# Performance work log

Hardware: AMD Instinct MI355X
Metric: run time of the kernel (lower is better)

## Reference

```python
import jax, jax.numpy as jnp
import numpy as np

H = 4        # nhead
TEMP = 0.1   # temperature
TOP_K = 5
SHAPE_EPS = 1e-5


def _ln(x, g, b):
    m = x.mean(-1, keepdims=True)
    v = ((x - m) ** 2).mean(-1, keepdims=True)
    return (x - m) / jnp.sqrt(v + SHAPE_EPS) * g + b


def _mha(x, Wqkv, bqkv, Wo, bo):
    B, L, D = x.shape
    Dh = D // H
    qkv = x @ Wqkv.T + bqkv                     # [B,L,3D]
    q, k, v = jnp.split(qkv, 3, axis=-1)
    q = q.reshape(B, L, H, Dh)
    k = k.reshape(B, L, H, Dh)
    v = v.reshape(B, L, H, Dh)
    att = jnp.einsum('bqhd,bkhd->bhqk', q, k) * (1.0 / np.sqrt(Dh))
    att = jax.nn.softmax(att, axis=-1)
    o = jnp.einsum('bhqk,bkhd->bqhd', att, v).reshape(B, L, D)
    return o @ Wo.T + bo


def _pattern_encoder(x, cls_token, Wqkv, bqkv, Wo, bo, ln1_g, ln1_b,
                     W1, b1, W2, b2, ln2_g, ln2_b, proj_W, proj_b, proj_g, proj_bb):
    B, L, D = x.shape
    h = jnp.concatenate([jnp.broadcast_to(cls_token, (B, 1, D)), x], axis=1)  # [B,L+1,D]
    for i in range(Wqkv.shape[0]):  # num_layers=2, post-norm (PyTorch default)
        a = _mha(h, Wqkv[i], bqkv[i], Wo[i], bo[i])
        h = _ln(h + a, ln1_g[i], ln1_b[i])
        f = jax.nn.gelu(h @ W1[i].T + b1[i], approximate=False) @ W2[i].T + b2[i]
        h = _ln(h + f, ln2_g[i], ln2_b[i])
    cls_out = h[:, 0, :]
    return _ln(cls_out @ proj_W.T + proj_b, proj_g, proj_bb)  # [B,d_repr]


def _value_encoder(xm, vW1, vb1, v_g, v_b, vW2, vb2):
    hh = _ln(xm @ vW1.T + vb1, v_g, v_b)
    return jax.nn.gelu(hh, approximate=False) @ vW2.T + vb2


def setup_inputs() -> dict:
    B, L, D, DR, N, P, NL = 64, 512, 512, 128, 10000, 96, 2
    key = jax.random.key(0)
    ks = jax.random.split(key, 16)
    sc = 0.02
    inp = {
        'query': jax.random.normal(ks[0], (B, L, D), jnp.float32),
        'memory_keys': jax.random.normal(ks[1], (N, DR), jnp.float32),
        'memory_values': jax.random.normal(ks[2], (N, P, D), jnp.float32),
        'cls_token': jax.random.normal(ks[3], (1, 1, D), jnp.float32) * sc,
        'Wqkv': jax.random.normal(ks[4], (NL, 3 * D, D), jnp.float32) * sc,
        'bqkv': jnp.zeros((NL, 3 * D), jnp.float32),
        'Wo': jax.random.normal(ks[5], (NL, D, D), jnp.float32) * sc,
        'bo': jnp.zeros((NL, D), jnp.float32),
        'ln1_g': jnp.ones((NL, D), jnp.float32),
        'ln1_b': jnp.zeros((NL, D), jnp.float32),
        'W1': jax.random.normal(ks[6], (NL, 2 * D, D), jnp.float32) * sc,
        'b1': jnp.zeros((NL, 2 * D), jnp.float32),
        'W2': jax.random.normal(ks[7], (NL, D, 2 * D), jnp.float32) * sc,
        'b2': jnp.zeros((NL, D), jnp.float32),
        'ln2_g': jnp.ones((NL, D), jnp.float32),
        'ln2_b': jnp.zeros((NL, D), jnp.float32),
        'proj_W': jax.random.normal(ks[8], (DR, D), jnp.float32) * sc,
        'proj_b': jnp.zeros((DR,), jnp.float32),
        'proj_g': jnp.ones((DR,), jnp.float32),
        'proj_bb': jnp.zeros((DR,), jnp.float32),
        'vW1': jax.random.normal(ks[9], (DR, D), jnp.float32) * sc,
        'vb1': jnp.zeros((DR,), jnp.float32),
        'v_g': jnp.ones((DR,), jnp.float32),
        'v_b': jnp.zeros((DR,), jnp.float32),
        'vW2': jax.random.normal(ks[10], (DR, DR), jnp.float32) * sc,
        'vb2': jnp.zeros((DR,), jnp.float32),
        'shape_w': jnp.float32(0.5),
    }
    return inp


def reference(query, memory_keys, memory_values, cls_token, Wqkv, bqkv, Wo, bo,
              ln1_g, ln1_b, W1, b1, W2, b2, ln2_g, ln2_b,
              proj_W, proj_b, proj_g, proj_bb, vW1, vb1, v_g, v_b, vW2, vb2, shape_w):
    q_repr = _pattern_encoder(query, cls_token, Wqkv, bqkv, Wo, bo, ln1_g, ln1_b,
                              W1, b1, W2, b2, ln2_g, ln2_b, proj_W, proj_b, proj_g, proj_bb)
    q_val = _value_encoder(query.mean(axis=1), vW1, vb1, v_g, v_b, vW2, vb2)
    qk = shape_w * q_repr + (1.0 - shape_w) * q_val              # [B,DR]
    # squared euclidean distance, expanded form (same math as sum((a-b)^2))
    d = ((qk ** 2).sum(-1)[:, None]
         - 2.0 * qk @ memory_keys.T
         + (memory_keys ** 2).sum(-1)[None, :])                  # [B,N]
    sim = -d / TEMP
    top_scores, top_idx = jax.lax.top_k(sim, TOP_K)              # [B,K]
    weights = jax.nn.softmax(top_scores, axis=-1)
    retrieved = memory_values[top_idx]                           # [B,K,P,D]
    return retrieved, weights
```

## Files before the change

### kernel.cpp

```cpp
#include <hip/hip_runtime.h>
#include <math.h>

#define B_    64
#define LQ    512
#define LC    513
#define DD    512
#define HH    4
#define DH    128
#define DRr   128
#define NKEYS 10000
#define PP    96
#define TOPK  5
#define MROWS (B_*LC)
#define VTSTRIDE 544

typedef __attribute__((ext_vector_type(8))) short short8v;
typedef __attribute__((ext_vector_type(4))) float f32x4;
typedef __attribute__((ext_vector_type(16))) float f32x16;

static __device__ __forceinline__ float gelu_exact(float x) {
    return 0.5f * x * (1.0f + erff(x * 0.70710678118654752440f));
}

static __device__ __forceinline__ unsigned short f2bf(float x) {
    union { float f; unsigned u; } v; v.f = x;
    unsigned r = v.u + 0x7fff + ((v.u >> 16) & 1);
    return (unsigned short)(r >> 16);
}
static __device__ __forceinline__ float bf2f(unsigned short h) {
    union { float f; unsigned u; } v; v.u = ((unsigned)h) << 16;
    return v.f;
}
static __device__ __forceinline__ void split_bf(float x, unsigned short& hi, unsigned short& lo) {
    hi = f2bf(x);
    lo = f2bf(x - bf2f(hi));
}

static __device__ __forceinline__ int xcd_swz(int orig, int nwg) {
    int xcd = orig & 7;
    int lid = orig >> 3;
    int q = nwg >> 3, r = nwg & 7;
    int base = (xcd < r) ? xcd * (q + 1) : r * (q + 1) + (xcd - r) * q;
    return base + lid;
}

static __device__ __forceinline__ void gload16(const unsigned short* g, unsigned short* l) {
    __builtin_amdgcn_global_load_lds(
        (const __attribute__((address_space(1))) unsigned*)g,
        (__attribute__((address_space(3))) unsigned*)l, 16, 0, 0);
}

__global__ __launch_bounds__(256)
void split_kernel(const float* __restrict__ x, unsigned short* __restrict__ hi,
                  unsigned short* __restrict__ lo, int n4)
{
    int i = blockIdx.x * blockDim.x + threadIdx.x;
    if (i >= n4) return;
    float4 v = ((const float4*)x)[i];
    unsigned short h0,h1,h2,h3,l0,l1,l2,l3;
    split_bf(v.x,h0,l0); split_bf(v.y,h1,l1); split_bf(v.z,h2,l2); split_bf(v.w,h3,l3);
    ((uint2*)hi)[i] = make_uint2((unsigned)h0 | ((unsigned)h1 << 16), (unsigned)h2 | ((unsigned)h3 << 16));
    ((uint2*)lo)[i] = make_uint2((unsigned)l0 | ((unsigned)l1 << 16), (unsigned)l2 | ((unsigned)l3 << 16));
}

__global__ __launch_bounds__(256)
void concat_cls(const float* __restrict__ query, const float* __restrict__ cls,
                float* __restrict__ h, unsigned short* __restrict__ h_hi,
                unsigned short* __restrict__ h_lo)
{
    int row = blockIdx.x * 4 + (threadIdx.x >> 6);
    int lane = threadIdx.x & 63;
    int b = row / LC, r = row - b * LC;
    const float* src = (r == 0) ? (cls + lane * 8)
                                : (query + ((size_t)b * LQ + (r - 1)) * DD + lane * 8);
    float4 v0 = *(const float4*)src;
    float4 v1 = *(const float4*)(src + 4);
    size_t o = (size_t)row * DD + lane * 8;
    *(float4*)(h + o) = v0;
    *(float4*)(h + o + 4) = v1;
    float vv[8] = {v0.x,v0.y,v0.z,v0.w,v1.x,v1.y,v1.z,v1.w};
    unsigned short hs[8], ls[8];
    #pragma unroll
    for (int i = 0; i < 8; i++) split_bf(vv[i], hs[i], ls[i]);
    uint4 hv, lv;
    hv.x = (unsigned)hs[0] | ((unsigned)hs[1] << 16);
    hv.y = (unsigned)hs[2] | ((unsigned)hs[3] << 16);
    hv.z = (unsigned)hs[4] | ((unsigned)hs[5] << 16);
    hv.w = (unsigned)hs[6] | ((unsigned)hs[7] << 16);
    lv.x = (unsigned)ls[0] | ((unsigned)ls[1] << 16);
    lv.y = (unsigned)ls[2] | ((unsigned)ls[3] << 16);
    lv.z = (unsigned)ls[4] | ((unsigned)ls[5] << 16);
    lv.w = (unsigned)ls[6] | ((unsigned)ls[7] << 16);
    *(uint4*)(h_hi + o) = hv;
    *(uint4*)(h_lo + o) = lv;
}

#define BM 128
#define BN 128
#define BK 32

#define MFMA32(a, b, c) __builtin_amdgcn_mfma_f32_32x32x16_bf16(a, b, c, 0, 0, 0)

template<int MODE>
__global__ __launch_bounds__(256)
void gemm3(const unsigned short* __restrict__ Ahi, const unsigned short* __restrict__ Alo,
           const unsigned short* __restrict__ Whi, const unsigned short* __restrict__ Wlo,
           const float* __restrict__ bias, const float* __restrict__ res,
           float* __restrict__ Cf, unsigned short* __restrict__ Chi,
           unsigned short* __restrict__ Clo, unsigned* __restrict__ Vix,
           int M, int N, int K, int NBN)
{
    __shared__ __align__(16) unsigned short POOL[16384];

    const int t = threadIdx.x;
    const int lane = t & 63, w = t >> 6;
    const int wr = w >> 1, wc = w & 1;
    const int wg = xcd_swz(blockIdx.x, gridDim.x);
    const int bm = wg / NBN, bn = wg - bm * NBN;
    const int row0 = bm * BM, col0 = bn * BN;

    const int srow = t >> 2;
    const int sg   = t & 3;
    const int glog = sg ^ (srow & 3);
    int ar0 = row0 + srow;      if (ar0 >= M) ar0 = M - 1;
    int ar1 = row0 + srow + 64; if (ar1 >= M) ar1 = M - 1;
    const size_t aoff0 = (size_t)ar0 * K + glog * 8;
    const size_t aoff1 = (size_t)ar1 * K + glog * 8;
    const size_t boff0 = (size_t)(col0 + srow) * K + glog * 8;
    const size_t boff1 = (size_t)(col0 + srow + 64) * K + glog * 8;
    const int ldso0 = t * 8;
    const int ldso1 = t * 8 + 2048;

    f32x16 acc[2][2];
    #pragma unroll
    for (int m = 0; m < 2; m++)
        #pragma unroll
        for (int n = 0; n < 2; n++)
            #pragma unroll
            for (int i = 0; i < 16; i++) acc[m][n][i] = 0.f;

    const int cl = lane & 31;
    const int kg = lane >> 5;
    const int cl3 = cl & 3;

    unsigned short* LAh = POOL;
    unsigned short* LAl = POOL + 4096;
    unsigned short* LBh = POOL + 8192;
    unsigned short* LBl = POOL + 12288;

    const int KT = K / BK;
    for (int kt = 0; kt < KT; kt++) {
        const int k0 = kt * BK;
        __syncthreads();
        gload16(Ahi + aoff0 + k0, &LAh[ldso0]);
        gload16(Ahi + aoff1 + k0, &LAh[ldso1]);
        gload16(Alo + aoff0 + k0, &LAl[ldso0]);
        gload16(Alo + aoff1 + k0, &LAl[ldso1]);
        gload16(Whi + boff0 + k0, &LBh[ldso0]);
        gload16(Whi + boff1 + k0, &LBh[ldso1]);
        gload16(Wlo + boff0 + k0, &LBl[ldso0]);
        gload16(Wlo + boff1 + k0, &LBl[ldso1]);
        __syncthreads();

        #pragma unroll
        for (int ks = 0; ks < 2; ks++) {
            const int blkswz = ((ks * 2 + kg) ^ cl3) * 8;
            short8v ah[2], al[2], bh[2], bl[2];
            #pragma unroll
            for (int m = 0; m < 2; m++) {
                int off = (wr * 64 + m * 32 + cl) * 32 + blkswz;
                ah[m] = *(const short8v*)&LAh[off];
                al[m] = *(const short8v*)&LAl[off];
            }
            #pragma unroll
            for (int n = 0; n < 2; n++) {
                int off = (wc * 64 + n * 32 + cl) * 32 + blkswz;
                bh[n] = *(const short8v*)&LBh[off];
                bl[n] = *(const short8v*)&LBl[off];
            }
            #pragma unroll
            for (int m = 0; m < 2; m++)
                #pragma unroll
                for (int n = 0; n < 2; n++) {
                    acc[m][n] = MFMA32(ah[m], bh[n], acc[m][n]);
                    acc[m][n] = MFMA32(al[m], bh[n], acc[m][n]);
                    acc[m][n] = MFMA32(ah[m], bl[n], acc[m][n]);
                }
        }
    }

    if (MODE == 3 && col0 >= 1024) {
        const int hh = (col0 - 1024) >> 7;
        unsigned* VS = (unsigned*)POOL;
        const int bb0 = row0 / LC;
        const int bound = (bb0 + 1) * LC;
        const int ddl = t >> 3, j0 = (t & 7) * 16;
        #pragma unroll
        for (int p = 0; p < 4; p++) {
            __syncthreads();
            if (wc == (p >> 1)) {
                const int ccl = col0 + wc * 64 + (p & 1) * 32 + cl;
                const float bcol = bias[ccl];
                #pragma unroll
                for (int m = 0; m < 2; m++) {
                    const int lrb = wr * 64 + m * 32 + 4 * kg;
                    #pragma unroll
                    for (int q = 0; q < 4; q++)
                        #pragma unroll
                        for (int r = 0; r < 4; r++) {
                            float v = ((p & 1) ? acc[m][1][q * 4 + r]
                                               : acc[m][0][q * 4 + r]) + bcol;
                            unsigned short hv, lv;
                            split_bf(v, hv, lv);
                            VS[cl * 129 + lrb + 8 * q + r] =
                                (unsigned)hv | ((unsigned)lv << 16);
                        }
                }
            }
            __syncthreads();
            long long vb0 = (long long)((bb0 * HH + hh) * DH + p * 32 + ddl) * VTSTRIDE
                            - (long long)bb0 * LC;
            long long vb1 = (long long)(((bb0 + 1) * HH + hh) * DH + p * 32 + ddl) * VTSTRIDE
                            - (long long)(bb0 + 1) * LC;
            #pragma unroll
            for (int j = 0; j < 16; j++) {
                int row = row0 + j0 + j;
                if (row < M) {
                    long long vi = (row < bound ? vb0 : vb1) + row;
                    Vix[vi] = VS[ddl * 129 + j0 + j];
                }
            }
        }
        return;
    }

    #pragma unroll
    for (int m = 0; m < 2; m++) {
        const int rb = row0 + wr * 64 + m * 32 + 4 * kg;
        #pragma unroll
        for (int n = 0; n < 2; n++) {
            const int cc = col0 + wc * 64 + n * 32 + cl;
            const float bcol = bias[cc];
            #pragma unroll
            for (int q = 0; q < 4; q++) {
                #pragma unroll
                for (int r = 0; r < 4; r++) {
                    int row = rb + 8 * q + r;
                    if (row < M) {
                        float v = acc[m][n][q * 4 + r] + bcol;
                        if (MODE == 1) v += res[(size_t)row * N + cc];
                        if (MODE == 2) {
                            v = gelu_exact(v);
                            unsigned short hv, lv;
                            split_bf(v, hv, lv);
                            Chi[(size_t)row * N + cc] = hv;
                            Clo[(size_t)row * N + cc] = lv;
                        } else if (MODE == 3) {
                            unsigned short hv, lv;
                            split_bf(v, hv, lv);
                            Chi[(size_t)row * 1024 + cc] = hv;
                            Clo[(size_t)row * 1024 + cc] = lv;
                        } else {
                            Cf[(size_t)row * N + cc] = v;
                        }
                    }
                }
            }
        }
    }
}

#define AQT 64
#define AKT 32
#define NKT2 17
#define MFMA16(a, b, c) __builtin_amdgcn_mfma_f32_16x16x32_bf16(a, b, c, 0, 0, 0)
__global__ __launch_bounds__(256)
void attn_mfma(const unsigned short* __restrict__ qkhi, const unsigned short* __restrict__ qklo,
               const unsigned* __restrict__ vtx,
               unsigned short* __restrict__ ohi, unsigned short* __restrict__ olo)
{
    __shared__ __align__(16) unsigned short SM[24064];
    #define KH(r,d) SM[(r)*136 + (d)]
    #define KL(r,d) SM[4352 + (r)*136 + (d)]
    #define VH(d,k) SM[8704 + (d)*40 + (k)]
    #define VL(d,k) SM[13824 + (d)*40 + (k)]
    #define PH(r,k) SM[18944 + (r)*40 + (k)]
    #define PL(r,k) SM[21504 + (r)*40 + (k)]
    #define OS(r,d) SM[(r)*136 + (d)]

    const int t = threadIdx.x;
    const int lane = t & 63, w = t >> 6;
    const int id = xcd_swz(blockIdx.x, gridDim.x);
    const int qt = id % 9;
    const int hb = id / 9;
    const int h = hb & 3, b = hb >> 2;
    const int q0 = qt * AQT;
    const int c = lane & 15, g = lane >> 4;
    const float SCALE = 0.08838834764831845f;

    short8v qh[4], ql[4];
    {
        int qrow = b * LC + q0 + w * 16 + c;
        if (qrow > MROWS - 1) qrow = MROWS - 1;
        const unsigned short* bh_ = qkhi + (size_t)qrow * 1024 + h * DH;
        const unsigned short* bl_ = qklo + (size_t)qrow * 1024 + h * DH;
        #pragma unroll
        for (int ks = 0; ks < 4; ks++) {
            qh[ks] = *(const short8v*)(bh_ + ks * 32 + g * 8);
            ql[ks] = *(const short8v*)(bl_ + ks * 32 + g * 8);
        }
    }

    float m_r[4], l_r[4];
    #pragma unroll
    for (int r = 0; r < 4; r++) { m_r[r] = -INFINITY; l_r[r] = 0.f; }
    f32x4 acc_o[8];
    #pragma unroll
    for (int n = 0; n < 8; n++) { acc_o[n][0]=0.f; acc_o[n][1]=0.f; acc_o[n][2]=0.f; acc_o[n][3]=0.f; }

    const int skr = t >> 3, skd = (t & 7) * 16;
    const int svd = t >> 1, svk = (t & 1) * 16;
    const unsigned short* kbase  = qkhi + 512 + h * DH + skd;
    const unsigned short* kbasel = qklo + 512 + h * DH + skd;
    const unsigned* vbase = vtx + ((size_t)((b * HH + h) * DH + svd)) * VTSTRIDE + svk;

    short8v rk0, rk1, rl0, rl1;
    uint4 rv0, rv1, rv2, rv3;
    {
        int krow = b * LC + skr; if (krow > MROWS - 1) krow = MROWS - 1;
        const unsigned short* kb  = kbase  + (size_t)krow * 1024;
        const unsigned short* kbl = kbasel + (size_t)krow * 1024;
        rk0 = *(const short8v*)kb;  rk1 = *(const short8v*)(kb + 8);
        rl0 = *(const short8v*)kbl; rl1 = *(const short8v*)(kbl + 8);
        rv0 = *(const uint4*)(vbase);
        rv1 = *(const uint4*)(vbase + 4);
        rv2 = *(const uint4*)(vbase + 8);
        rv3 = *(const uint4*)(vbase + 12);
    }

    for (int kt = 0; kt < NKT2; kt++) {
        __builtin_amdgcn_s_barrier();
        *(short8v*)&KH(skr, skd)     = rk0;
        *(short8v*)&KH(skr, skd + 8) = rk1;
        *(short8v*)&KL(skr, skd)     = rl0;
        *(short8v*)&KL(skr, skd + 8) = rl1;
        {
            uint4 hA, hB, lA, lB;
            hA.x = (rv0.x & 0xffffu) | (rv0.y << 16);
            hA.y = (rv0.z & 0xffffu) | (rv0.w << 16);
            hA.z = (rv1.x & 0xffffu) | (rv1.y << 16);
            hA.w = (rv1.z & 0xffffu) | (rv1.w << 16);
            hB.x = (rv2.x & 0xffffu) | (rv2.y << 16);
            hB.y = (rv2.z & 0xffffu) | (rv2.w << 16);
            hB.z = (rv3.x & 0xffffu) | (rv3.y << 16);
            hB.w = (rv3.z & 0xffffu) | (rv3.w << 16);
            lA.x = (rv0.x >> 16) | (rv0.y & 0xffff0000u);
            lA.y = (rv0.z >> 16) | (rv0.w & 0xffff0000u);
            lA.z = (rv1.x >> 16) | (rv1.y & 0xffff0000u);
            lA.w = (rv1.z >> 16) | (rv1.w & 0xffff0000u);
            lB.x = (rv2.x >> 16) | (rv2.y & 0xffff0000u);
            lB.y = (rv2.z >> 16) | (rv2.w & 0xffff0000u);
            lB.z = (rv3.x >> 16) | (rv3.y & 0xffff0000u);
            lB.w = (rv3.z >> 16) | (rv3.w & 0xffff0000u);
            *(uint4*)&VH(svd, svk)     = hA;
            *(uint4*)&VH(svd, svk + 8) = hB;
            *(uint4*)&VL(svd, svk)     = lA;
            *(uint4*)&VL(svd, svk + 8) = lB;
        }
        if (kt + 1 < NKT2) {
            int krow = b * LC + (kt + 1) * AKT + skr;
            if (krow > MROWS - 1) krow = MROWS - 1;
            const unsigned short* kb  = kbase  + (size_t)krow * 1024;
            const unsigned short* kbl = kbasel + (size_t)krow * 1024;
            rk0 = *(const short8v*)kb;  rk1 = *(const short8v*)(kb + 8);
            rl0 = *(const short8v*)kbl; rl1 = *(const short8v*)(kbl + 8);
            const unsigned* vb = vbase + (kt + 1) * AKT;
            rv0 = *(const uint4*)(vb);
            rv1 = *(const uint4*)(vb + 4);
            rv2 = *(const uint4*)(vb + 8);
            rv3 = *(const uint4*)(vb + 12);
        }
        asm volatile("s_waitcnt lgkmcnt(0)" ::: "memory");
        __builtin_amdgcn_s_barrier();
        __builtin_amdgcn_sched_barrier(0);

        f32x4 s[2];
        s[0][0]=s[0][1]=s[0][2]=s[0][3]=0.f;
        s[1][0]=s[1][1]=s[1][2]=s[1][3]=0.f;
        __builtin_amdgcn_s_setprio(1);
        #pragma unroll
        for (int n = 0; n < 2; n++) {
            #pragma unroll
            for (int ks = 0; ks < 4; ks++) {
                short8v kh = *(const short8v*)&KH(n * 16 + c, ks * 32 + g * 8);
                short8v kl = *(const short8v*)&KL(n * 16 + c, ks * 32 + g * 8);
                s[n] = MFMA16(qh[ks], kh, s[n]);
                s[n] = MFMA16(ql[ks], kh, s[n]);
                s[n] = MFMA16(qh[ks], kl, s[n]);
            }
        }
        __builtin_amdgcn_s_setprio(0);

        #pragma unroll
        for (int n = 0; n < 2; n++) {
            bool oob = (kt * 32 + n * 16 + c) >= LC;
            #pragma unroll
            for (int r = 0; r < 4; r++) {
                float sv = s[n][r] * SCALE;
                s[n][r] = oob ? -INFINITY : sv;
            }
        }

        float alpha[4], p0v[4], p1v[4];
        #pragma unroll
        for (int r = 0; r < 4; r++) {
            float rm = fmaxf(s[0][r], s[1][r]);
            #pragma unroll
            for (int off = 1; off < 16; off <<= 1) rm = fmaxf(rm, __shfl_xor(rm, off));
            float mn = fmaxf(m_r[r], rm);
            float p0 = expf(s[0][r] - mn);
            float p1 = expf(s[1][r] - mn);
            float ts = p0 + p1;
            #pragma unroll
            for (int off = 1; off < 16; off <<= 1) ts += __shfl_xor(ts, off);
            float al = expf(m_r[r] - mn);
            m_r[r] = mn;
            l_r[r] = al * l_r[r] + ts;
            alpha[r] = al;
            p0v[r] = p0; p1v[r] = p1;
        }

        #pragma unroll
        for (int n = 0; n < 8; n++)
            #pragma unroll
            for (int r = 0; r < 4; r++) acc_o[n][r] *= alpha[r];

        #pragma unroll
        for (int r = 0; r < 4; r++) {
            unsigned short ph, pl;
            split_bf(p0v[r], ph, pl);
            PH(w * 16 + g * 4 + r, c) = ph;
            PL(w * 16 + g * 4 + r, c) = pl;
            split_bf(p1v[r], ph, pl);
            PH(w * 16 + g * 4 + r, 16 + c) = ph;
            PL(w * 16 + g * 4 + r, 16 + c) = pl;
        }
        short8v pah = *(const short8v*)&PH(w * 16 + c, g * 8);
        short8v pal = *(const short8v*)&PL(w * 16 + c, g * 8);
        __builtin_amdgcn_s_setprio(1);
        #pragma unroll
        for (int n = 0; n < 8; n++) {
            short8v vh = *(const short8v*)&VH(n * 16 + c, g * 8);
            short8v vl = *(const short8v*)&VL(n * 16 + c, g * 8);
            acc_o[n] = MFMA16(pah, vh, acc_o[n]);
            acc_o[n] = MFMA16(pal, vh, acc_o[n]);
            acc_o[n] = MFMA16(pah, vl, acc_o[n]);
        }
        __builtin_amdgcn_s_setprio(0);
    }

    float inv[4];
    #pragma unroll
    for (int r = 0; r < 4; r++) inv[r] = 1.0f / l_r[r];

    const int orow = t >> 2, oc0 = (t & 3) * 32;
    #pragma unroll
    for (int pass = 0; pass < 2; pass++) {
        __syncthreads();
        #pragma unroll
        for (int n = 0; n < 8; n++)
            #pragma unroll
            for (int r = 0; r < 4; r++) {
                float v = acc_o[n][r] * inv[r];
                unsigned short hv, lv;
                split_bf(v, hv, lv);
                OS(w * 16 + g * 4 + r, n * 16 + c) = pass ? lv : hv;
            }
        __syncthreads();
        int grow = q0 + orow;
        if (grow < LC) {
            unsigned short* dst = (pass ? olo : ohi) + ((size_t)(b * LC + grow)) * DD + h * DH + oc0;
            #pragma unroll
            for (int u = 0; u < 4; u++)
                *(short8v*)(dst + u * 8) = *(const short8v*)&OS(orow, oc0 + u * 8);
        }
    }
    #undef KH
    #undef KL
    #undef VH
    #undef VL
    #undef PH
    #undef PL
    #undef OS
}

__global__ __launch_bounds__(256)
void ln512(const float* __restrict__ X, const float* __restrict__ g,
           const float* __restrict__ bb, float* __restrict__ Y,
           unsigned short* __restrict__ Yhi, unsigned short* __restrict__ Ylo)
{
    int row = blockIdx.x * 4 + (threadIdx.x >> 6);
    int lane = threadIdx.x & 63;
    const float* x = X + (size_t)row * DD + lane * 8;
    float4 v0 = *(const float4*)x;
    float4 v1 = *(const float4*)(x + 4);
    float vv[8] = {v0.x,v0.y,v0.z,v0.w,v1.x,v1.y,v1.z,v1.w};
    float s = 0.f;
    #pragma unroll
    for (int i = 0; i < 8; i++) s += vv[i];
    #pragma unroll
    for (int off = 1; off < 64; off <<= 1) s += __shfl_xor(s, off);
    float mean = s * (1.0f / 512.0f);
    float d[8], s2 = 0.f;
    #pragma unroll
    for (int i = 0; i < 8; i++) { d[i] = vv[i] - mean; s2 += d[i] * d[i]; }
    #pragma unroll
    for (int off = 1; off < 64; off <<= 1) s2 += __shfl_xor(s2, off);
    float var = s2 * (1.0f / 512.0f);
    float rstd = 1.0f / sqrtf(var + 1e-5f);
    float4 g0 = *(const float4*)(g + lane * 8);
    float4 g1 = *(const float4*)(g + lane * 8 + 4);
    float4 b0 = *(const float4*)(bb + lane * 8);
    float4 b1 = *(const float4*)(bb + lane * 8 + 4);
    float gg[8] = {g0.x,g0.y,g0.z,g0.w,g1.x,g1.y,g1.z,g1.w};
    float bv[8] = {b0.x,b0.y,b0.z,b0.w,b1.x,b1.y,b1.z,b1.w};
    float ov[8];
    unsigned short hs[8], ls[8];
    #pragma unroll
    for (int i = 0; i < 8; i++) {
        ov[i] = d[i] * rstd * gg[i] + bv[i];
        split_bf(ov[i], hs[i], ls[i]);
    }
    size_t o = (size_t)row * DD + lane * 8;
    *(float4*)(Y + o)     = make_float4(ov[0], ov[1], ov[2], ov[3]);
    *(float4*)(Y + o + 4) = make_float4(ov[4], ov[5], ov[6], ov[7]);
    uint4 hv, lv;
    hv.x = (unsigned)hs[0] | ((unsigned)hs[1] << 16);
    hv.y = (unsigned)hs[2] | ((unsigned)hs[3] << 16);
    hv.z = (unsigned)hs[4] | ((unsigned)hs[5] << 16);
    hv.w = (unsigned)hs[6] | ((unsigned)hs[7] << 16);
    lv.x = (unsigned)ls[0] | ((unsigned)ls[1] << 16);
    lv.y = (unsigned)ls[2] | ((unsigned)ls[3] << 16);
    lv.z = (unsigned)ls[4] | ((unsigned)ls[5] << 16);
    lv.w = (unsigned)ls[6] | ((unsigned)ls[7] << 16);
    *(uint4*)(Yhi + o) = hv;
    *(uint4*)(Ylo + o) = lv;
}

__global__ __launch_bounds__(128)
void mean_part(const float* __restrict__ query, float* __restrict__ part)
{
    int b = blockIdx.x, ch = blockIdx.y, t = threadIdx.x;
    const float* base = query + ((size_t)b * LQ + ch * 64) * DD + t * 4;
    float ax = 0.f, ay = 0.f, az = 0.f, aw = 0.f;
    for (int l = 0; l < 64; l++) {
        float4 v = *(const float4*)(base + (size_t)l * DD);
        ax += v.x; ay += v.y; az += v.z; aw += v.w;
    }
    *(float4*)(part + ((size_t)(b * 8 + ch)) * DD + t * 4) = make_float4(ax, ay, az, aw);
}

__global__ __launch_bounds__(128)
void mean_fin(const float* __restrict__ part, float* __restrict__ xm)
{
    int b = blockIdx.x, t = threadIdx.x;
    float ax = 0.f, ay = 0.f, az = 0.f, aw = 0.f;
    #pragma unroll
    for (int ch = 0; ch < 8; ch++) {
        float4 v = *(const float4*)(part + ((size_t)(b * 8 + ch)) * DD + t * 4);
        ax += v.x; ay += v.y; az += v.z; aw += v.w;
    }
    *(float4*)(xm + (size_t)b * DD + t * 4) =
        make_float4(ax * (1.f/512.f), ay * (1.f/512.f), az * (1.f/512.f), aw * (1.f/512.f));
}

static __device__ __forceinline__ float block128_sum(float x, float* red, int t) {
    #pragma unroll
    for (int off = 1; off < 64; off <<= 1) x += __shfl_xor(x, off);
    if ((t & 63) == 0) red[t >> 6] = x;
    __syncthreads();
    float r = red[0] + red[1];
    __syncthreads();
    return r;
}

__global__ __launch_bounds__(128)
void proj_ln(const float* __restrict__ h, const float* __restrict__ pW, const float* __restrict__ pb,
             const float* __restrict__ pg, const float* __restrict__ pbb, float* __restrict__ q_repr)
{
    __shared__ float xs[DD];
    __shared__ float red[2];
    int b = blockIdx.x, t = threadIdx.x;
    *(float4*)&xs[t * 4] = *(const float4*)(h + (size_t)(b * LC) * DD + t * 4);
    __syncthreads();
    const float* w = pW + (size_t)t * DD;
    float acc = pb[t];
    for (int k = 0; k < DD; k += 4) {
        float4 a = *(const float4*)&xs[k];
        float4 ww = *(const float4*)(w + k);
        acc += a.x * ww.x + a.y * ww.y + a.z * ww.z + a.w * ww.w;
    }
    float mean = block128_sum(acc, red, t) * (1.f / 128.f);
    float dx = acc - mean;
    float var = block128_sum(dx * dx, red, t) * (1.f / 128.f);
    float rstd = 1.0f / sqrtf(var + 1e-5f);
    q_repr[(size_t)b * DRr + t] = dx * rstd * pg[t] + pbb[t];
}

__global__ __launch_bounds__(128)
void venc(const float* __restrict__ xm, const float* __restrict__ vW1, const float* __restrict__ vb1,
          const float* __restrict__ vg, const float* __restrict__ vb,
          const float* __restrict__ vW2, const float* __restrict__ vb2,
          float* __restrict__ q_val)
{
    __shared__ float xs[DD];
    __shared__ float hg[DRr];
    __shared__ float red[2];
    int b = blockIdx.x, t = threadIdx.x;
    *(float4*)&xs[t * 4] = *(const float4*)(xm + (size_t)b * DD + t * 4);
    __syncthreads();
    const float* w = vW1 + (size_t)t * DD;
    float acc = vb1[t];
    for (int k = 0; k < DD; k += 4) {
        float4 a = *(const float4*)&xs[k];
        float4 ww = *(const float4*)(w + k);
        acc += a.x * ww.x + a.y * ww.y + a.z * ww.z + a.w * ww.w;
    }
    float mean = block128_sum(acc, red, t) * (1.f / 128.f);
    float dx = acc - mean;
    float var = block128_sum(dx * dx, red, t) * (1.f / 128.f);
    float rstd = 1.0f / sqrtf(var + 1e-5f);
    float hn = dx * rstd * vg[t] + vb[t];
    hg[t] = gelu_exact(hn);
    __syncthreads();
    const float* w2 = vW2 + (size_t)t * DRr;
    float acc2 = vb2[t];
    for (int k = 0; k < DRr; k += 4) {
        float4 a = *(const float4*)&hg[k];
        float4 ww = *(const float4*)(w2 + k);
        acc2 += a.x * ww.x + a.y * ww.y + a.z * ww.z + a.w * ww.w;
    }
    q_val[(size_t)b * DRr + t] = acc2;
}

__global__ void combine_qk(const float* __restrict__ qr, const float* __restrict__ qv,
                           const float* __restrict__ swp, float* __restrict__ qk)
{
    int i = blockIdx.x * blockDim.x + threadIdx.x;
    if (i < B_ * DRr) {
        float sw = swp[0];
        qk[i] = sw * qr[i] + (1.f - sw) * qv[i];
    }
}

#define SIMCH 10
__global__ __launch_bounds__(256)
void sim_kernel(const float* __restrict__ qk, const float* __restrict__ mkeys, float* __restrict__ sim)
{
    __shared__ float qs[DRr];
    int b = blockIdx.x, ch = blockIdx.y, t = threadIdx.x;
    if (t < DRr) qs[t] = qk[(size_t)b * DRr + t];
    __syncthreads();
    float qn = 0.f;
    #pragma unroll 8
    for (int i = 0; i < DRr; i++) qn += qs[i] * qs[i];
    int n0 = ch * (NKEYS / SIMCH), n1 = n0 + (NKEYS / SIMCH);
    for (int n = n0 + t; n < n1; n += 256) {
        const float* kr = mkeys + (size_t)n * DRr;
        float dot = 0.f, kn = 0.f;
        #pragma unroll 8
        for (int i = 0; i < DRr; i += 4) {
            float4 kv = *(const float4*)(kr + i);
            dot += qs[i] * kv.x + qs[i + 1] * kv.y + qs[i + 2] * kv.z + qs[i + 3] * kv.w;
            kn  += kv.x * kv.x + kv.y * kv.y + kv.z * kv.z + kv.w * kv.w;
        }
        float d = qn - 2.f * dot + kn;
        sim[(size_t)b * NKEYS + n] = -d / 0.1f;
    }
}

static __device__ __forceinline__ void topk_insert(float* v, int* id, float x, int n) {
    bool better = (x > v[TOPK - 1]) || (x == v[TOPK - 1] && n < id[TOPK - 1]);
    if (better) {
        v[TOPK - 1] = x; id[TOPK - 1] = n;
        #pragma unroll
        for (int k = TOPK - 1; k > 0; k--) {
            bool sw = (v[k] > v[k - 1]) || (v[k] == v[k - 1] && id[k] < id[k - 1]);
            if (!sw) break;
            float tv = v[k]; v[k] = v[k - 1]; v[k - 1] = tv;
            int ti = id[k]; id[k] = id[k - 1]; id[k - 1] = ti;
        }
    }
}

__global__ __launch_bounds__(256)
void topk_kernel(const float* __restrict__ sim, int* __restrict__ topidx, float* __restrict__ wout)
{
    __shared__ float sv[256][TOPK];
    __shared__ int   si[256][TOPK];
    int b = blockIdx.x, t = threadIdx.x;
    float v[TOPK]; int id[TOPK];
    #pragma unroll
    for (int k = 0; k < TOPK; k++) { v[k] = -INFINITY; id[k] = 0x7fffffff; }
    for (int n = t; n < NKEYS; n += 256) {
        topk_insert(v, id, sim[(size_t)b * NKEYS + n], n);
    }
    #pragma unroll
    for (int k = 0; k < TOPK; k++) { sv[t][k] = v[k]; si[t][k] = id[k]; }
    for (int strd = 128; strd >= 1; strd >>= 1) {
        __syncthreads();
        if (t < strd) {
            #pragma unroll
            for (int k = 0; k < TOPK; k++) topk_insert(v, id, sv[t + strd][k], si[t + strd][k]);
            #pragma unroll
            for (int k = 0; k < TOPK; k++) { sv[t][k] = v[k]; si[t][k] = id[k]; }
        }
    }
    if (t == 0) {
        float m = v[0];
        float e[TOPK]; float sum = 0.f;
        #pragma unroll
        for (int k = 0; k < TOPK; k++) { e[k] = expf(v[k] - m); sum += e[k]; }
        #pragma unroll
        for (int k = 0; k < TOPK; k++) {
            wout[(size_t)b * TOPK + k] = e[k] / sum;
            topidx[b * TOPK + k] = id[k];
        }
    }
}

__global__ __launch_bounds__(128)
void gather_kernel(const float* __restrict__ mv, const int* __restrict__ topidx, float* __restrict__ out)
{
    int blk = blockIdx.x;
    int b = blk / (TOPK * PP);
    int rem = blk - b * (TOPK * PP);
    int k = rem / PP;
    int p = rem - k * PP;
    int idx = topidx[b * TOPK + k];
    const float4* src = (const float4*)(mv + ((size_t)idx * PP + p) * DD);
    float4* dst = (float4*)(out + (size_t)blk * DD);
    dst[threadIdx.x] = src[threadIdx.x];
}

extern "C" void kernel_launch(void* const* d_in, const int* in_sizes, int n_in,
                              void* d_out, int out_size, void* d_ws, size_t ws_size,
                              hipStream_t stream) {
    const float* query = (const float*)d_in[0];
    const float* mkeys = (const float*)d_in[1];
    const float* mvals = (const float*)d_in[2];
    const float* cls   = (const float*)d_in[3];
    const float* Wqkv  = (const float*)d_in[4];
    const float* bqkv  = (const float*)d_in[5];
    const float* Wo    = (const float*)d_in[6];
    const float* bo    = (const float*)d_in[7];
    const float* ln1g  = (const float*)d_in[8];
    const float* ln1b  = (const float*)d_in[9];
    const float* W1    = (const float*)d_in[10];
    const float* b1    = (const float*)d_in[11];
    const float* W2    = (const float*)d_in[12];
    const float* b2    = (const float*)d_in[13];
    const float* ln2g  = (const float*)d_in[14];
    const float* ln2b  = (const float*)d_in[15];
    const float* pW    = (const float*)d_in[16];
    const float* pb    = (const float*)d_in[17];
    const float* pg    = (const float*)d_in[18];
    const float* pbb   = (const float*)d_in[19];
    const float* vW1   = (const float*)d_in[20];
    const float* vb1   = (const float*)d_in[21];
    const float* vg    = (const float*)d_in[22];
    const float* vb    = (const float*)d_in[23];
    const float* vW2   = (const float*)d_in[24];
    const float* vb2   = (const float*)d_in[25];
    const float* swp   = (const float*)d_in[26];
    float* out = (float*)d_out;

    float* ws    = (float*)d_ws;
    float* h     = ws;
    float* preln = h + (size_t)MROWS * DD;
    unsigned short* h_hi  = (unsigned short*)(preln + (size_t)MROWS * DD);
    unsigned short* h_lo  = h_hi  + (size_t)MROWS * DD;
    unsigned short* mid_hi = h_lo + (size_t)MROWS * DD;
    unsigned short* mid_lo = mid_hi + (size_t)MROWS * 1024;
    unsigned short* qkhi  = mid_lo + (size_t)MROWS * 1024;
    unsigned short* qklo  = qkhi  + (size_t)MROWS * 1024;
    unsigned* vtx         = (unsigned*)(qklo + (size_t)MROWS * 1024);
    unsigned short* wq_hi = (unsigned short*)(vtx + (size_t)32768 * VTSTRIDE);
    unsigned short* wq_lo = wq_hi + (size_t)2 * 1536 * DD;
    unsigned short* wo_hi = wq_lo + (size_t)2 * 1536 * DD;
    unsigned short* wo_lo = wo_hi + (size_t)2 * DD * DD;
    unsigned short* w1_hi = wo_lo + (size_t)2 * DD * DD;
    unsigned short* w1_lo = w1_hi + (size_t)2 * 1024 * DD;
    unsigned short* w2_hi = w1_lo + (size_t)2 * 1024 * DD;
    unsigned short* w2_lo = w2_hi + (size_t)2 * DD * 1024;
    float* xm   = (float*)(w2_lo + (size_t)2 * DD * 1024);
    float* qval = xm   + (size_t)B_ * DD;
    float* qrep = qval + (size_t)B_ * DRr;
    float* qkc  = qrep + (size_t)B_ * DRr;
    float* simb = qkc  + (size_t)B_ * DRr;
    int*   tidx = (int*)(simb + (size_t)B_ * NKEYS);
    float* mpart = (float*)(tidx + 512);
    (void)ws_size; (void)in_sizes; (void)n_in; (void)out_size;

    {
        int n4;
        n4 = 2 * 1536 * DD / 4;
        split_kernel<<<(n4 + 255) / 256, 256, 0, stream>>>(Wqkv, wq_hi, wq_lo, n4);
        n4 = 2 * DD * DD / 4;
        split_kernel<<<(n4 + 255) / 256, 256, 0, stream>>>(Wo, wo_hi, wo_lo, n4);
        n4 = 2 * 1024 * DD / 4;
        split_kernel<<<(n4 + 255) / 256, 256, 0, stream>>>(W1, w1_hi, w1_lo, n4);
        n4 = 2 * DD * 1024 / 4;
        split_kernel<<<(n4 + 255) / 256, 256, 0, stream>>>(W2, w2_hi, w2_lo, n4);
    }

    concat_cls<<<MROWS / 4, 256, 0, stream>>>(query, cls, h, h_hi, h_lo);

    for (int l = 0; l < 2; l++) {
        const unsigned short* wqh = wq_hi + (size_t)l * 1536 * DD;
        const unsigned short* wql = wq_lo + (size_t)l * 1536 * DD;
        const unsigned short* woh = wo_hi + (size_t)l * DD * DD;
        const unsigned short* wol = wo_lo + (size_t)l * DD * DD;
        const unsigned short* w1h = w1_hi + (size_t)l * 1024 * DD;
        const unsigned short* w1l = w1_lo + (size_t)l * 1024 * DD;
        const unsigned short* w2h = w2_hi + (size_t)l * DD * 1024;
        const unsigned short* w2l = w2_lo + (size_t)l * DD * 1024;
        const float* bq  = bqkv + (size_t)l * 1536;
        const float* bol = bo   + (size_t)l * DD;
        const float* g1  = ln1g + (size_t)l * DD;
        const float* be1 = ln1b + (size_t)l * DD;
        const float* b1l = b1   + (size_t)l * 1024;
        const float* b2l = b2   + (size_t)l * DD;
        const float* g2  = ln2g + (size_t)l * DD;
        const float* be2 = ln2b + (size_t)l * DD;

        gemm3<3><<<257 * 12, 256, 0, stream>>>(h_hi, h_lo, wqh, wql, bq, nullptr,
                                               nullptr, qkhi, qklo, vtx,
                                               MROWS, 1536, DD, 12);
        attn_mfma<<<9 * HH * B_, 256, 0, stream>>>(qkhi, qklo, vtx, h_hi, h_lo);
        gemm3<1><<<257 * 4, 256, 0, stream>>>(h_hi, h_lo, woh, wol, bol, h,
                                              preln, nullptr, nullptr, nullptr,
                                              MROWS, DD, DD, 4);
        ln512<<<MROWS / 4, 256, 0, stream>>>(preln, g1, be1, h, h_hi, h_lo);
        gemm3<2><<<257 * 8, 256, 0, stream>>>(h_hi, h_lo, w1h, w1l, b1l, nullptr,
                                              nullptr, mid_hi, mid_lo, nullptr,
                                              MROWS, 1024, DD, 8);
        gemm3<1><<<257 * 4, 256, 0, stream>>>(mid_hi, mid_lo, w2h, w2l, b2l, h,
                                              preln, nullptr, nullptr, nullptr,
                                              MROWS, DD, 1024, 4);
        ln512<<<MROWS / 4, 256, 0, stream>>>(preln, g2, be2, h, h_hi, h_lo);
    }

    proj_ln<<<B_, 128, 0, stream>>>(h, pW, pb, pg, pbb, qrep);
    mean_part<<<dim3(B_, 8), 128, 0, stream>>>(query, mpart);
    mean_fin<<<B_, 128, 0, stream>>>(mpart, xm);
    venc<<<B_, 128, 0, stream>>>(xm, vW1, vb1, vg, vb, vW2, vb2, qval);
    combine_qk<<<(B_ * DRr + 255) / 256, 256, 0, stream>>>(qrep, qval, swp, qkc);
    sim_kernel<<<dim3(B_, SIMCH), 256, 0, stream>>>(qkc, mkeys, simb);
    topk_kernel<<<B_, 256, 0, stream>>>(simb, tidx, out + (size_t)B_ * TOPK * PP * DD);
    gather_kernel<<<B_ * TOPK * PP, 128, 0, stream>>>(mvals, tidx, out);
}
```

Before: 2.421 ms.

## Drop fp32 residual copy of hidden state; fuse similarity with top-k

The float32 copy of the hidden state is no longer stored. Residual adds, the projection input and the LayerNorm outputs now rebuild it from the existing bf16 hi/lo split pair, which removes a 67 MB fp32 write per LayerNorm and the fp32 residual reads. Attention output moves to separate ao buffers so h_hi/h_lo can serve as the residual. The similarity and top-k kernels are merged, so the sim buffer disappears, but only 64 blocks now scan all 10000 keys, which reduces parallelism in that stage.

```diff
diff --git a/kernel.cpp b/kernel.cpp
--- a/kernel.cpp
+++ b/kernel.cpp
@@ -65,8 +65,7 @@
 
 __global__ __launch_bounds__(256)
 void concat_cls(const float* __restrict__ query, const float* __restrict__ cls,
-                float* __restrict__ h, unsigned short* __restrict__ h_hi,
-                unsigned short* __restrict__ h_lo)
+                unsigned short* __restrict__ h_hi, unsigned short* __restrict__ h_lo)
 {
     int row = blockIdx.x * 4 + (threadIdx.x >> 6);
     int lane = threadIdx.x & 63;
@@ -76,8 +75,6 @@
     float4 v0 = *(const float4*)src;
     float4 v1 = *(const float4*)(src + 4);
     size_t o = (size_t)row * DD + lane * 8;
-    *(float4*)(h + o) = v0;
-    *(float4*)(h + o + 4) = v1;
     float vv[8] = {v0.x,v0.y,v0.z,v0.w,v1.x,v1.y,v1.z,v1.w};
     unsigned short hs[8], ls[8];
     #pragma unroll
@@ -105,7 +102,8 @@
 __global__ __launch_bounds__(256)
 void gemm3(const unsigned short* __restrict__ Ahi, const unsigned short* __restrict__ Alo,
            const unsigned short* __restrict__ Whi, const unsigned short* __restrict__ Wlo,
-           const float* __restrict__ bias, const float* __restrict__ res,
+           const float* __restrict__ bias,
+           const unsigned short* __restrict__ Rhi, const unsigned short* __restrict__ Rlo,
            float* __restrict__ Cf, unsigned short* __restrict__ Chi,
            unsigned short* __restrict__ Clo, unsigned* __restrict__ Vix,
            int M, int N, int K, int NBN)
@@ -248,7 +246,10 @@
                     int row = rb + 8 * q + r;
                     if (row < M) {
                         float v = acc[m][n][q * 4 + r] + bcol;
-                        if (MODE == 1) v += res[(size_t)row * N + cc];
+                        if (MODE == 1) {
+                            size_t ri = (size_t)row * N + cc;
+                            v += bf2f(Rhi[ri]) + bf2f(Rlo[ri]);
+                        }
                         if (MODE == 2) {
                             v = gelu_exact(v);
                             unsigned short hv, lv;
@@ -496,7 +497,7 @@
 
 __global__ __launch_bounds__(256)
 void ln512(const float* __restrict__ X, const float* __restrict__ g,
-           const float* __restrict__ bb, float* __restrict__ Y,
+           const float* __restrict__ bb,
            unsigned short* __restrict__ Yhi, unsigned short* __restrict__ Ylo)
 {
     int row = blockIdx.x * 4 + (threadIdx.x >> 6);
@@ -524,16 +525,13 @@
     float4 b1 = *(const float4*)(bb + lane * 8 + 4);
     float gg[8] = {g0.x,g0.y,g0.z,g0.w,g1.x,g1.y,g1.z,g1.w};
     float bv[8] = {b0.x,b0.y,b0.z,b0.w,b1.x,b1.y,b1.z,b1.w};
-    float ov[8];
     unsigned short hs[8], ls[8];
     #pragma unroll
     for (int i = 0; i < 8; i++) {
-        ov[i] = d[i] * rstd * gg[i] + bv[i];
-        split_bf(ov[i], hs[i], ls[i]);
+        float ov = d[i] * rstd * gg[i] + bv[i];
+        split_bf(ov, hs[i], ls[i]);
     }
     size_t o = (size_t)row * DD + lane * 8;
-    *(float4*)(Y + o)     = make_float4(ov[0], ov[1], ov[2], ov[3]);
-    *(float4*)(Y + o + 4) = make_float4(ov[4], ov[5], ov[6], ov[7]);
     uint4 hv, lv;
     hv.x = (unsigned)hs[0] | ((unsigned)hs[1] << 16);
     hv.y = (unsigned)hs[2] | ((unsigned)hs[3] << 16);
@@ -585,13 +583,22 @@
 }
 
 __global__ __launch_bounds__(128)
-void proj_ln(const float* __restrict__ h, const float* __restrict__ pW, const float* __restrict__ pb,
+void proj_ln(const unsigned short* __restrict__ Hhi, const unsigned short* __restrict__ Hlo,
+             const float* __restrict__ pW, const float* __restrict__ pb,
              const float* __restrict__ pg, const float* __restrict__ pbb, float* __restrict__ q_repr)
 {
     __shared__ float xs[DD];
     __shared__ float red[2];
     int b = blockIdx.x, t = threadIdx.x;
-    *(float4*)&xs[t * 4] = *(const float4*)(h + (size_t)(b * LC) * DD + t * 4);
+    {
+        size_t base = ((size_t)(b * LC)) * DD;
+        uint2 hw = ((const uint2*)(Hhi + base))[t];
+        uint2 lw = ((const uint2*)(Hlo + base))[t];
+        xs[t * 4 + 0] = bf2f((unsigned short)hw.x) + bf2f((unsigned short)lw.x);
+        xs[t * 4 + 1] = bf2f((unsigned short)(hw.x >> 16)) + bf2f((unsigned short)(lw.x >> 16));
+        xs[t * 4 + 2] = bf2f((unsigned short)hw.y) + bf2f((unsigned short)lw.y);
+        xs[t * 4 + 3] = bf2f((unsigned short)(hw.y >> 16)) + bf2f((unsigned short)(lw.y >> 16));
+    }
     __syncthreads();
     const float* w = pW + (size_t)t * DD;
     float acc = pb[t];
@@ -653,19 +660,38 @@
     }
 }
 
-#define SIMCH 10
+static __device__ __forceinline__ void topk_insert(float* v, int* id, float x, int n) {
+    bool better = (x > v[TOPK - 1]) || (x == v[TOPK - 1] && n < id[TOPK - 1]);
+    if (better) {
+        v[TOPK - 1] = x; id[TOPK - 1] = n;
+        #pragma unroll
+        for (int k = TOPK - 1; k > 0; k--) {
+            bool sw = (v[k] > v[k - 1]) || (v[k] == v[k - 1] && id[k] < id[k - 1]);
+            if (!sw) break;
+            float tv = v[k]; v[k] = v[k - 1]; v[k - 1] = tv;
+            int ti = id[k]; id[k] = id[k - 1]; id[k - 1] = ti;
+        }
+    }
+}
+
 __global__ __launch_bounds__(256)
-void sim_kernel(const float* __restrict__ qk, const float* __restrict__ mkeys, float* __restrict__ sim)
+void sim_topk(const float* __restrict__ qk, const float* __restrict__ mkeys,
+              int* __restrict__ topidx, float* __restrict__ wout)
 {
     __shared__ float qs[DRr];
-    int b = blockIdx.x, ch = blockIdx.y, t = threadIdx.x;
+    __shared__ float sv[256][TOPK];
+    __shared__ int   si[256][TOPK];
+    int b = blockIdx.x, t = threadIdx.x;
     if (t < DRr) qs[t] = qk[(size_t)b * DRr + t];
     __syncthreads();
     float qn = 0.f;
     #pragma unroll 8
     for (int i = 0; i < DRr; i++) qn += qs[i] * qs[i];
-    int n0 = ch * (NKEYS / SIMCH), n1 = n0 + (NKEYS / SIMCH);
-    for (int n = n0 + t; n < n1; n += 256) {
+
+    float v[TOPK]; int id[TOPK];
+    #pragma unroll
+    for (int k = 0; k < TOPK; k++) { v[k] = -INFINITY; id[k] = 0x7fffffff; }
+    for (int n = t; n < NKEYS; n += 256) {
         const float* kr = mkeys + (size_t)n * DRr;
         float dot = 0.f, kn = 0.f;
         #pragma unroll 8
@@ -675,35 +701,7 @@
             kn  += kv.x * kv.x + kv.y * kv.y + kv.z * kv.z + kv.w * kv.w;
         }
         float d = qn - 2.f * dot + kn;
-        sim[(size_t)b * NKEYS + n] = -d / 0.1f;
-    }
-}
-
-static __device__ __forceinline__ void topk_insert(float* v, int* id, float x, int n) {
-    bool better = (x > v[TOPK - 1]) || (x == v[TOPK - 1] && n < id[TOPK - 1]);
-    if (better) {
-        v[TOPK - 1] = x; id[TOPK - 1] = n;
-        #pragma unroll
-        for (int k = TOPK - 1; k > 0; k--) {
-            bool sw = (v[k] > v[k - 1]) || (v[k] == v[k - 1] && id[k] < id[k - 1]);
-            if (!sw) break;
-            float tv = v[k]; v[k] = v[k - 1]; v[k - 1] = tv;
-            int ti = id[k]; id[k] = id[k - 1]; id[k - 1] = ti;
-        }
-    }
-}
-
-__global__ __launch_bounds__(256)
-void topk_kernel(const float* __restrict__ sim, int* __restrict__ topidx, float* __restrict__ wout)
-{
-    __shared__ float sv[256][TOPK];
-    __shared__ int   si[256][TOPK];
-    int b = blockIdx.x, t = threadIdx.x;
-    float v[TOPK]; int id[TOPK];
-    #pragma unroll
-    for (int k = 0; k < TOPK; k++) { v[k] = -INFINITY; id[k] = 0x7fffffff; }
-    for (int n = t; n < NKEYS; n += 256) {
-        topk_insert(v, id, sim[(size_t)b * NKEYS + n], n);
+        topk_insert(v, id, -d / 0.1f, n);
     }
     #pragma unroll
     for (int k = 0; k < TOPK; k++) { sv[t][k] = v[k]; si[t][k] = id[k]; }
@@ -776,11 +774,12 @@
     float* out = (float*)d_out;
 
     float* ws    = (float*)d_ws;
-    float* h     = ws;
-    float* preln = h + (size_t)MROWS * DD;
+    float* preln = ws;
     unsigned short* h_hi  = (unsigned short*)(preln + (size_t)MROWS * DD);
     unsigned short* h_lo  = h_hi  + (size_t)MROWS * DD;
-    unsigned short* mid_hi = h_lo + (size_t)MROWS * DD;
+    unsigned short* ao_hi = h_lo  + (size_t)MROWS * DD;
+    unsigned short* ao_lo = ao_hi + (size_t)MROWS * DD;
+    unsigned short* mid_hi = ao_lo + (size_t)MROWS * DD;
     unsigned short* mid_lo = mid_hi + (size_t)MROWS * 1024;
     unsigned short* qkhi  = mid_lo + (size_t)MROWS * 1024;
     unsigned short* qklo  = qkhi  + (size_t)MROWS * 1024;
@@ -797,8 +796,7 @@
     float* qval = xm   + (size_t)B_ * DD;
     float* qrep = qval + (size_t)B_ * DRr;
     float* qkc  = qrep + (size_t)B_ * DRr;
-    float* simb = qkc  + (size_t)B_ * DRr;
-    int*   tidx = (int*)(simb + (size_t)B_ * NKEYS);
+    int*   tidx = (int*)(qkc + (size_t)B_ * DRr);
     float* mpart = (float*)(tidx + 512);
     (void)ws_size; (void)in_sizes; (void)n_in; (void)out_size;
 
@@ -814,7 +812,7 @@
         split_kernel<<<(n4 + 255) / 256, 256, 0, stream>>>(W2, w2_hi, w2_lo, n4);
     }
 
-    concat_cls<<<MROWS / 4, 256, 0, stream>>>(query, cls, h, h_hi, h_lo);
+    concat_cls<<<MROWS / 4, 256, 0, stream>>>(query, cls, h_hi, h_lo);
 
     for (int l = 0; l < 2; l++) {
         const unsigned short* wqh = wq_hi + (size_t)l * 1536 * DD;
@@ -834,29 +832,32 @@
         const float* g2  = ln2g + (size_t)l * DD;
         const float* be2 = ln2b + (size_t)l * DD;
 
-        gemm3<3><<<257 * 12, 256, 0, stream>>>(h_hi, h_lo, wqh, wql, bq, nullptr,
+        gemm3<3><<<257 * 12, 256, 0, stream>>>(h_hi, h_lo, wqh, wql, bq,
+                                               nullptr, nullptr,
                                                nullptr, qkhi, qklo, vtx,
                                                MROWS, 1536, DD, 12);
-        attn_mfma<<<9 * HH * B_, 256, 0, stream>>>(qkhi, qklo, vtx, h_hi, h_lo);
-        gemm3<1><<<257 * 4, 256, 0, stream>>>(h_hi, h_lo, woh, wol, bol, h,
+        attn_mfma<<<9 * HH * B_, 256, 0, stream>>>(qkhi, qklo, vtx, ao_hi, ao_lo);
+        gemm3<1><<<257 * 4, 256, 0, stream>>>(ao_hi, ao_lo, woh, wol, bol,
+                                              h_hi, h_lo,
                                               preln, nullptr, nullptr, nullptr,
                                               MROWS, DD, DD, 4);
-        ln512<<<MROWS / 4, 256, 0, stream>>>(preln, g1, be1, h, h_hi, h_lo);
-        gemm3<2><<<257 * 8, 256, 0, stream>>>(h_hi, h_lo, w1h, w1l, b1l, nullptr,
+        ln512<<<MROWS / 4, 256, 0, stream>>>(preln, g1, be1, h_hi, h_lo);
+        gemm3<2><<<257 * 8, 256, 0, stream>>>(h_hi, h_lo, w1h, w1l, b1l,
+                                              nullptr, nullptr,
                                               nullptr, mid_hi, mid_lo, nullptr,
                                               MROWS, 1024, DD, 8);
-        gemm3<1><<<257 * 4, 256, 0, stream>>>(mid_hi, mid_lo, w2h, w2l, b2l, h,
+        gemm3<1><<<257 * 4, 256, 0, stream>>>(mid_hi, mid_lo, w2h, w2l, b2l,
+                                              h_hi, h_lo,
                                               preln, nullptr, nullptr, nullptr,
                                               MROWS, DD, 1024, 4);
-        ln512<<<MROWS / 4, 256, 0, stream>>>(preln, g2, be2, h, h_hi, h_lo);
-    }
-
-    proj_ln<<<B_, 128, 0, stream>>>(h, pW, pb, pg, pbb, qrep);
+        ln512<<<MROWS / 4, 256, 0, stream>>>(preln, g2, be2, h_hi, h_lo);
+    }
+
+    proj_ln<<<B_, 128, 0, stream>>>(h_hi, h_lo, pW, pb, pg, pbb, qrep);
     mean_part<<<dim3(B_, 8), 128, 0, stream>>>(query, mpart);
     mean_fin<<<B_, 128, 0, stream>>>(mpart, xm);
     venc<<<B_, 128, 0, stream>>>(xm, vW1, vb1, vg, vb, vW2, vb2, qval);
     combine_qk<<<(B_ * DRr + 255) / 256, 256, 0, stream>>>(qrep, qval, swp, qkc);
-    sim_kernel<<<dim3(B_, SIMCH), 256, 0, stream>>>(qkc, mkeys, simb);
-    topk_kernel<<<B_, 256, 0, stream>>>(simb, tidx, out + (size_t)B_ * TOPK * PP * DD);
+    sim_topk<<<B_, 256, 0, stream>>>(qkc, mkeys, tidx, out + (size_t)B_ * TOPK * PP * DD);
     gather_kernel<<<B_ * TOPK * PP, 128, 0, stream>>>(mvals, tidx, out);
 }
```

Measured after the change: 2.532 ms. 1.05x slower.
